# Kernel optimization log

Measured on AMD Instinct MI355X. Metric: run time of the kernel, lower is better.

The kernel has to match this reference:

```python
import jax, jax.numpy as jnp
import numpy as np

B, L = 1024, 1024
NCAT, NNUM = 20, 10
CAT_BUCKETS, SEQ_VOCAB = 100000, 50000
E, A, H, QH = 32, 128, 256, 256
TOPK = 30


def _init(key, shape, scale=0.02):
    return scale * jax.random.normal(key, shape, dtype=jnp.float32)


def setup_inputs() -> dict:
    key = jax.random.key(0)
    ks = jax.random.split(key, 24)
    z = lambda *s: jnp.zeros(s, dtype=jnp.float32)
    return {
        "cats": jax.random.randint(ks[0], (B, NCAT), 0, CAT_BUCKETS + 1),
        "nums": jax.random.normal(ks[1], (B, NNUM), dtype=jnp.float32),
        "seqs": jax.random.randint(ks[2], (B, L), 0, SEQ_VOCAB + 1),
        "tgt_ids": jax.random.randint(ks[3], (B,), 0, CAT_BUCKETS + 1),
        "cat_emb": _init(ks[4], (CAT_BUCKETS + 1, E)),
        "seq_emb": _init(ks[5], (SEQ_VOCAB + 1, E)),
        "Wnum": _init(ks[6], (NNUM, E)), "bnum": z(E),
        "Wq": _init(ks[7], (E, A)), "Wk": _init(ks[8], (E, A)), "Wv": _init(ks[9], (E, A)),
        "Wo": _init(ks[10], (A, E)), "bo": z(E),
        "Wpool": _init(ks[11], (NCAT * E, E)), "bpool": z(E),
        "Wmlp": _init(ks[12], (4 * E, H)), "bmlp": z(H),
        "q1_W1": _init(ks[13], (H, QH)), "q1_b1": z(QH),
        "q1_W2": _init(ks[14], (H, QH)), "q1_b2": z(QH),
        "q1_Wp": _init(ks[15], (QH, H)), "q1_bp": z(H),
        "q2_W1": _init(ks[16], (H, QH)), "q2_b1": z(QH),
        "q2_W2": _init(ks[17], (H, QH)), "q2_b2": z(QH),
        "q2_Wp": _init(ks[18], (QH, H)), "q2_bp": z(H),
        "Wout": _init(ks[19], (H, 1)), "bout": z(1),
    }


def _qnn(x, W1, b1, W2, b2, Wp, bp):
    # Quadratic neural block (QIN-style): Hadamard product of two linear maps,
    # projected back with a residual connection. Dropout is identity in eval.
    quad = (x @ W1 + b1) * (x @ W2 + b2)
    return x + quad @ Wp + bp


def reference(cats, nums, seqs, tgt_ids, cat_emb, seq_emb, Wnum, bnum, Wq, Wk, Wv,
              Wo, bo, Wpool, bpool, Wmlp, bmlp,
              q1_W1, q1_b1, q1_W2, q1_b2, q1_Wp, q1_bp,
              q2_W1, q2_b1, q2_W2, q2_b2, q2_Wp, q2_bp, Wout, bout):
    cat_e = cat_emb[cats]                                   # [B, NCAT, E]
    cat_pool = cat_e.reshape(cat_e.shape[0], -1) @ Wpool + bpool   # [B, E]
    num_e = nums @ Wnum + bnum                              # [B, E]
    tgt_e = cat_emb[tgt_ids]                                # [B, E] (tgt_emb shares cat_emb)
    seq_e = seq_emb[seqs]                                   # [B, L, E]

    q = tgt_e @ Wq                                          # [B, A]
    k = seq_e @ Wk                                          # [B, L, A]
    v = seq_e @ Wv                                          # [B, L, A]
    scores = jnp.einsum('ba,bla->bl', q, k) / jnp.sqrt(jnp.float32(A))

    # top-k + scatter mask + masked softmax == softmax over the top-k scores,
    # scattered implicitly via gather of the selected values.
    vals, idx = jax.lax.top_k(scores, TOPK)                 # [B, TOPK]
    w = jax.nn.softmax(vals, axis=1)                        # [B, TOPK]
    v_sel = jnp.take_along_axis(v, idx[:, :, None], axis=1)  # [B, TOPK, A]
    interest = jnp.einsum('bk,bka->ba', w, v_sel) @ Wo + bo  # [B, E]

    fused = jnp.concatenate([tgt_e, interest, cat_pool, num_e], axis=1)  # [B, 4E]
    h = jax.nn.relu(fused @ Wmlp + bmlp)                    # [B, H], dropout=eval
    h = _qnn(h, q1_W1, q1_b1, q1_W2, q1_b2, q1_Wp, q1_bp)
    h = _qnn(h, q2_W1, q2_b1, q2_W2, q2_b2, q2_Wp, q2_bp)
    return (h @ Wout + bout)[:, 0]                          # [B]
```

## Files before the change

kernel.cpp:

```cpp
#include <hip/hip_runtime.h>
#include <hip/hip_fp16.h>

#define B_ 1024
#define L_ 1024
#define NCAT_ 20
#define NNUM_ 10
#define E_ 32
#define A_ 128
#define H_ 256
#define TOPK_ 30
#define INV_SQRT_A 0.08838834764831845f

typedef _Float16 half8 __attribute__((ext_vector_type(8)));
typedef float f32x4 __attribute__((ext_vector_type(4)));

__device__ __forceinline__ unsigned sortable(float f) {
    unsigned u = __float_as_uint(f);
    return (u & 0x80000000u) ? ~u : (u | 0x80000000u);
}
__device__ __forceinline__ float unsortable(unsigned s) {
    unsigned u = (s & 0x80000000u) ? (s ^ 0x80000000u) : ~s;
    return __uint_as_float(u);
}
__device__ __forceinline__ half8 cvt_h8(const float4 u, const float4 v) {
    half8 a;
    a[0] = (_Float16)u.x; a[1] = (_Float16)u.y;
    a[2] = (_Float16)u.z; a[3] = (_Float16)u.w;
    a[4] = (_Float16)v.x; a[5] = (_Float16)v.y;
    a[6] = (_Float16)v.z; a[7] = (_Float16)v.w;
    return a;
}

#define K1_GRID 1356
__global__ __launch_bounds__(256) void fused_prep_kernel(
    const int* __restrict__ cats, const float* __restrict__ nums,
    const int* __restrict__ tgt_ids, const float* __restrict__ cat_emb,
    const float* __restrict__ Wnum, const float* __restrict__ bnum,
    const float* __restrict__ Wq, const float* __restrict__ Wk,
    const float* __restrict__ Wv, const float* __restrict__ Wo,
    const float* __restrict__ Wpool, const float* __restrict__ bpool,
    const float* __restrict__ seq_emb, const float* __restrict__ Wmlp,
    const float* __restrict__ q1W1, const float* __restrict__ q1W2,
    const float* __restrict__ q1Wp,
    const float* __restrict__ q2W1, const float* __restrict__ q2W2,
    const float* __restrict__ q2Wp,
    float* __restrict__ p_out, float* __restrict__ fused, float* __restrict__ M,
    int* __restrict__ cnt, __half2* __restrict__ seq_h2,
    __half* __restrict__ WmlpT,
    __half* __restrict__ W1T1, __half* __restrict__ W2T1, __half* __restrict__ WpT1,
    __half* __restrict__ W1T2, __half* __restrict__ W2T2, __half* __restrict__ WpT2)
{
    const int blk = blockIdx.x;
    const int t = threadIdx.x;

    if (blk < 256) {
        __shared__ float ce[4][NCAT_ * E_];
        __shared__ float tg[4][E_];
        __shared__ float nm[4][NNUM_];
        __shared__ float qs[4][A_];
        __shared__ float part[8][4][E_];
        const int r0 = blk * 4;

        for (int idx = t; idx < 640; idx += 256) {
            const int q = idx >> 3, f4 = idx & 7;
            const int row = q / 20, cat = q % 20;
            const int tok = cats[(r0 + row) * NCAT_ + cat];
            ((float4*)&ce[row][cat * 32])[f4] =
                ((const float4*)(cat_emb + (size_t)tok * 32))[f4];
        }
        if (t < 32) {
            const int row = t >> 3, f4 = t & 7;
            const int tok = tgt_ids[r0 + row];
            ((float4*)&tg[row][0])[f4] =
                ((const float4*)(cat_emb + (size_t)tok * 32))[f4];
        }
        if (t >= 64 && t < 104) {
            const int x = t - 64;
            nm[x / 10][x % 10] = nums[(r0 + x / 10) * NNUM_ + x % 10];
        }
        __syncthreads();

        {
            const int w = t >> 6, lane = t & 63;
            float q0 = 0.f, q1 = 0.f;
#pragma unroll
            for (int e = 0; e < E_; ++e) {
                float te = tg[w][e];
                q0 += te * Wq[e * A_ + lane];
                q1 += te * Wq[e * A_ + lane + 64];
            }
            qs[w][lane] = q0; qs[w][lane + 64] = q1;
        }

        {
            const int iseg = t >> 5;
            const int row = (t >> 3) & 3;
            const int c0 = (t & 7) * 4;
            float4 acc = make_float4(0.f, 0.f, 0.f, 0.f);
            const int i0 = iseg * 80;
            for (int i = i0; i < i0 + 80; ++i) {
                float4 wv = *(const float4*)(Wpool + i * 32 + c0);
                acc.x += ce[row][i] * wv.x; acc.y += ce[row][i] * wv.y;
                acc.z += ce[row][i] * wv.z; acc.w += ce[row][i] * wv.w;
            }
            *(float4*)&part[iseg][row][c0] = acc;
        }
        __syncthreads();

        if (t < 128) {
            const int row = t >> 5, c = t & 31;
            const int b = r0 + row;
            float s = bpool[c];
#pragma unroll
            for (int g = 0; g < 8; ++g) s += part[g][row][c];
            fused[b * 128 + 64 + c] = s;
            fused[b * 128 + c] = tg[row][c];

            float ne = bnum[c];
#pragma unroll
            for (int n = 0; n < NNUM_; ++n) ne += nm[row][n] * Wnum[n * 32 + c];
            fused[b * 128 + 96 + c] = ne;

            float pv = 0.f;
#pragma unroll 8
            for (int a = 0; a < A_; ++a) pv += Wk[c * A_ + a] * qs[row][a];
            p_out[b * 32 + c] = pv;
        }
        return;
    }

    if (blk < 1280) {
        int x = (blk - 256) * 256 + t;
        for (; x < 800016; x += 1024 * 256) {
            float2 v = ((const float2*)seq_emb)[x];
            seq_h2[x] = __float22half2_rn(v);
        }
        return;
    }

    if (blk < 1284) {
        if (blk == 1280 && t < 64) cnt[t] = 0;
        const int o = (blk - 1280) * 256 + t;
        const int j = o >> 5, e = o & 31;
        float sm = 0.f;
#pragma unroll 8
        for (int a = 0; a < A_; ++a) sm += Wv[j * A_ + a] * Wo[a * E_ + e];
        M[o] = sm;
        return;
    }

    {
        int c = (blk - 1284) * 256 + t;
        for (; c < 53248; c += 72 * 256) {
            const float* src; __half* dst;
            int n, k0, K;
            if (c < 4096) {
                n = c >> 4; k0 = (c & 15) << 3; K = 128;
                src = Wmlp; dst = WmlpT;
            } else {
                const int c2 = c - 4096;
                const int m = c2 >> 13, idx = c2 & 8191;
                n = idx >> 5; k0 = (idx & 31) << 3; K = 256;
                switch (m) {
                    case 0: src = q1W1; dst = W1T1; break;
                    case 1: src = q1W2; dst = W2T1; break;
                    case 2: src = q1Wp; dst = WpT1; break;
                    case 3: src = q2W1; dst = W1T2; break;
                    case 4: src = q2W2; dst = W2T2; break;
                    default: src = q2Wp; dst = WpT2; break;
                }
            }
            float v[8];
#pragma unroll
            for (int i = 0; i < 8; ++i) v[i] = src[(size_t)(k0 + i) * 256 + n];
            float4 wq;
            __half2* hp = (__half2*)&wq;
            hp[0] = __float22half2_rn(make_float2(v[0], v[1]));
            hp[1] = __float22half2_rn(make_float2(v[2], v[3]));
            hp[2] = __float22half2_rn(make_float2(v[4], v[5]));
            hp[3] = __float22half2_rn(make_float2(v[6], v[7]));
            *(float4*)(dst + (size_t)n * K + k0) = wq;
        }
    }
}

#define RM 4
#define GR 16
#define HSP 260
#define TSP 264
__global__ __launch_bounds__(512) void score_mlp_kernel(
    const int* __restrict__ seqs, const __half* __restrict__ seq_h,
    const float* __restrict__ seq_emb, const float* __restrict__ p,
    const float* __restrict__ M, const float* __restrict__ bo,
    float* __restrict__ fused, int* __restrict__ cnt,
    const __half* __restrict__ WmlpT, const float* __restrict__ bmlp,
    const __half* __restrict__ W1T1, const __half* __restrict__ W2T1,
    const __half* __restrict__ WpT1,
    const float* __restrict__ b11, const float* __restrict__ b12,
    const float* __restrict__ b1p,
    const __half* __restrict__ W1T2, const __half* __restrict__ W2T2,
    const __half* __restrict__ WpT2,
    const float* __restrict__ b21, const float* __restrict__ b22,
    const float* __restrict__ b2p,
    const float* __restrict__ Wout, const float* __restrict__ bout,
    float* __restrict__ out)
{
    const int b0 = blockIdx.x * RM;
    const int tid = threadIdx.x;

    __shared__ float sc[RM][L_];
    __shared__ float ps[RM][E_];
    __shared__ float sw[RM][32];
    __shared__ int   stok[RM][32];
    __shared__ float hs[GR][HSP];
    __shared__ __half ts_h[GR][TSP];
    __shared__ int doml;

    if (tid < RM * 32)
        ps[tid >> 5][tid & 31] = p[(b0 + (tid >> 5)) * 32 + (tid & 31)];
    __syncthreads();

    {
        const int row = tid >> 7;
        const int s = tid & 127;
        const int bb = b0 + row;
#pragma unroll
        for (int jj = 0; jj < 4; ++jj) {
            const int l1 = jj * 256 + s;
            const int l2 = l1 + 128;
            const int tok1 = seqs[bb * L_ + l1];
            const int tok2 = seqs[bb * L_ + l2];
            float4 buf[2][4];
            const float4* r1 = (const float4*)(seq_h + (size_t)tok1 * 32);
            const float4* r2 = (const float4*)(seq_h + (size_t)tok2 * 32);
#pragma unroll
            for (int i = 0; i < 4; ++i) buf[0][i] = r1[i];
#pragma unroll
            for (int i = 0; i < 4; ++i) buf[1][i] = r2[i];

            float acc0 = 0.f, acc1 = 0.f;
#pragma unroll
            for (int i = 0; i < 4; ++i) {
                const __half2* h1 = (const __half2*)&buf[0][i];
                const __half2* h2 = (const __half2*)&buf[1][i];
#pragma unroll
                for (int u = 0; u < 4; ++u) {
                    float2 f1 = __half22float2(h1[u]);
                    float2 f2 = __half22float2(h2[u]);
                    acc0 += f1.x * ps[row][i * 8 + 2 * u] + f1.y * ps[row][i * 8 + 2 * u + 1];
                    acc1 += f2.x * ps[row][i * 8 + 2 * u] + f2.y * ps[row][i * 8 + 2 * u + 1];
                }
            }
            sc[row][l1] = acc0 * INV_SQRT_A;
            sc[row][l2] = acc1 * INV_SQRT_A;
        }
    }
    __syncthreads();

    if (tid < RM * 64) {
        const int w = tid >> 6;
        const int lane = tid & 63;
        const int bb = b0 + w;

        unsigned long long key[16];
#pragma unroll
        for (int j = 0; j < 16; ++j) {
            const int l = j * 64 + lane;
            key[j] = ((unsigned long long)sortable(sc[w][l]) << 10)
                   | (unsigned)(1023 - l);
        }
#pragma unroll
        for (int a = 0; a < 15; ++a)
#pragma unroll
            for (int j = 0; j < 15 - a; ++j) {
                const bool swp = key[j] < key[j + 1];
                const unsigned long long hi = swp ? key[j + 1] : key[j];
                const unsigned long long lo = swp ? key[j] : key[j + 1];
                key[j] = hi; key[j + 1] = lo;
            }

        float myv = -1e30f; int myl = 0;
        unsigned long long front = key[0];
        for (int k = 0; k < TOPK_; ++k) {
            unsigned long long wk = front;
#pragma unroll
            for (int off = 32; off > 0; off >>= 1) {
                unsigned long long o = __shfl_xor(wk, off);
                if (o > wk) wk = o;
            }
            if (lane == k) {
                myv = unsortable((unsigned)(wk >> 10));
                myl = 1023 - (int)(wk & 1023);
            }
            if (front == wk) {
#pragma unroll
                for (int j = 0; j < 15; ++j) key[j] = key[j + 1];
                key[15] = 0ULL;
                front = key[0];
            }
        }

        float m = myv;
#pragma unroll
        for (int off = 32; off > 0; off >>= 1) m = fmaxf(m, __shfl_xor(m, off));
        float e = (lane < TOPK_) ? expf(myv - m) : 0.f;
        float s = e;
#pragma unroll
        for (int off = 32; off > 0; off >>= 1) s += __shfl_xor(s, off);
        if (lane < TOPK_) {
            sw[w][lane]   = e / s;
            stok[w][lane] = seqs[bb * L_ + myl];
        }

        if (lane < E_) {
            float acc = 0.f;
#pragma unroll
            for (int k = 0; k < TOPK_; ++k)
                acc += sw[w][k] * seq_emb[(size_t)stok[w][k] * 32 + lane];
            sc[w][lane] = acc;
        }
        if (lane < E_) {
            float acc = bo[lane];
#pragma unroll
            for (int j = 0; j < E_; ++j) acc += sc[w][j] * M[j * E_ + lane];
            fused[bb * 128 + 32 + lane] = acc;
        }
    }
    __syncthreads();

    if (tid == 0) {
        __threadfence();
        const int g = blockIdx.x >> 2;
        const int old = atomicAdd(&cnt[g], 1);
        doml = (old == 3) ? 1 : 0;
        if (old == 3) __threadfence();
    }
    __syncthreads();
    if (!doml) return;

    const int r0m = (blockIdx.x >> 2) * GR;
    const int w = tid >> 6;
    const int l = tid & 63;
    const int lr = l & 15;
    const int lk = l >> 4;
    const int n0 = w * 32;

    f32x4 hC0, hC1;
    const f32x4 zf = {0.f, 0.f, 0.f, 0.f};

    {
        half8 ax[4];
        const float* xrow = fused + (size_t)(r0m + lr) * 128 + lk * 8;
#pragma unroll
        for (int ks = 0; ks < 4; ++ks) {
            float4 u = *(const float4*)(xrow + ks * 32);
            float4 v = *(const float4*)(xrow + ks * 32 + 4);
            ax[ks] = cvt_h8(u, v);
        }
#pragma unroll
        for (int t = 0; t < 2; ++t) {
            f32x4 c = zf;
            const __half* wb = WmlpT + (size_t)(n0 + 16 * t + lr) * 128 + lk * 8;
#pragma unroll
            for (int ks = 0; ks < 4; ++ks) {
                half8 b = *(const half8*)(wb + ks * 32);
                c = __builtin_amdgcn_mfma_f32_16x16x32_f16(ax[ks], b, c, 0, 0, 0);
            }
            const int j = n0 + 16 * t + lr;
            const float bm = bmlp[j];
#pragma unroll
            for (int r = 0; r < 4; ++r) {
                float vv = fmaxf(c[r] + bm, 0.f);
                if (t == 0) hC0[r] = vv; else hC1[r] = vv;
                hs[4 * lk + r][j] = vv;
            }
        }
    }
    __syncthreads();

#pragma unroll
    for (int q = 0; q < 2; ++q) {
        const __half* W1T = q ? W1T2 : W1T1;
        const __half* W2T = q ? W2T2 : W2T1;
        const __half* WpT = q ? WpT2 : WpT1;
        const float* bb1 = q ? b21 : b11;
        const float* bb2 = q ? b22 : b12;
        const float* bbp = q ? b2p : b1p;

        half8 ah[8];
#pragma unroll
        for (int ks = 0; ks < 8; ++ks) {
            const float* hr = &hs[lr][ks * 32 + lk * 8];
            float4 u = *(const float4*)hr;
            float4 v = *(const float4*)(hr + 4);
            ah[ks] = cvt_h8(u, v);
        }
#pragma unroll
        for (int t = 0; t < 2; ++t) {
            f32x4 t1 = zf, t2 = zf;
            const __half* w1 = W1T + (size_t)(n0 + 16 * t + lr) * 256 + lk * 8;
            const __half* w2 = W2T + (size_t)(n0 + 16 * t + lr) * 256 + lk * 8;
#pragma unroll
            for (int ks = 0; ks < 8; ++ks) {
                half8 b1 = *(const half8*)(w1 + ks * 32);
                t1 = __builtin_amdgcn_mfma_f32_16x16x32_f16(ah[ks], b1, t1, 0, 0, 0);
                half8 b2 = *(const half8*)(w2 + ks * 32);
                t2 = __builtin_amdgcn_mfma_f32_16x16x32_f16(ah[ks], b2, t2, 0, 0, 0);
            }
            const int j = n0 + 16 * t + lr;
            const float v1 = bb1[j], v2 = bb2[j];
#pragma unroll
            for (int r = 0; r < 4; ++r) {
                float tv = (t1[r] + v1) * (t2[r] + v2);
                ts_h[4 * lk + r][j] = __float2half_rn(tv);
            }
        }
        __syncthreads();

        half8 pa[8];
#pragma unroll
        for (int ks = 0; ks < 8; ++ks)
            pa[ks] = *(const half8*)&ts_h[lr][ks * 32 + lk * 8];
#pragma unroll
        for (int t = 0; t < 2; ++t) {
            f32x4 c = (t == 0) ? hC0 : hC1;
            const __half* wp = WpT + (size_t)(n0 + 16 * t + lr) * 256 + lk * 8;
#pragma unroll
            for (int ks = 0; ks < 8; ++ks) {
                half8 b = *(const half8*)(wp + ks * 32);
                c = __builtin_amdgcn_mfma_f32_16x16x32_f16(pa[ks], b, c, 0, 0, 0);
            }
            const int j = n0 + 16 * t + lr;
            const float bp = bbp[j];
#pragma unroll
            for (int r = 0; r < 4; ++r) {
                float vv = c[r] + bp;
                if (t == 0) hC0[r] = vv; else hC1[r] = vv;
                hs[4 * lk + r][j] = vv;
            }
        }
        __syncthreads();
    }

    {
        const int i = tid >> 5;
        const int seg = tid & 31;
        const int cb = seg * 8;
        float psum = 0.f;
#pragma unroll
        for (int u = 0; u < 8; ++u) psum += hs[i][cb + u] * Wout[cb + u];
#pragma unroll
        for (int off = 16; off > 0; off >>= 1) psum += __shfl_xor(psum, off);
        if (seg == 0) out[r0m + i] = psum + bout[0];
    }
}

extern "C" void kernel_launch(void* const* d_in, const int* in_sizes, int n_in,
                              void* d_out, int out_size, void* d_ws, size_t ws_size,
                              hipStream_t stream) {
    const int*   cats    = (const int*)d_in[0];
    const float* nums    = (const float*)d_in[1];
    const int*   seqs    = (const int*)d_in[2];
    const int*   tgt_ids = (const int*)d_in[3];
    const float* cat_emb = (const float*)d_in[4];
    const float* seq_emb = (const float*)d_in[5];
    const float* Wnum    = (const float*)d_in[6];
    const float* bnum    = (const float*)d_in[7];
    const float* Wq      = (const float*)d_in[8];
    const float* Wk      = (const float*)d_in[9];
    const float* Wv      = (const float*)d_in[10];
    const float* Wo      = (const float*)d_in[11];
    const float* bo      = (const float*)d_in[12];
    const float* Wpool   = (const float*)d_in[13];
    const float* bpool   = (const float*)d_in[14];
    const float* Wmlp    = (const float*)d_in[15];
    const float* bmlp    = (const float*)d_in[16];
    const float* q1_W1   = (const float*)d_in[17];
    const float* q1_b1   = (const float*)d_in[18];
    const float* q1_W2   = (const float*)d_in[19];
    const float* q1_b2   = (const float*)d_in[20];
    const float* q1_Wp   = (const float*)d_in[21];
    const float* q1_bp   = (const float*)d_in[22];
    const float* q2_W1   = (const float*)d_in[23];
    const float* q2_b1   = (const float*)d_in[24];
    const float* q2_W2   = (const float*)d_in[25];
    const float* q2_b2   = (const float*)d_in[26];
    const float* q2_Wp   = (const float*)d_in[27];
    const float* q2_bp   = (const float*)d_in[28];
    const float* Wout    = (const float*)d_in[29];
    const float* bout    = (const float*)d_in[30];

    float* ws = (float*)d_ws;
    float*   p       = ws;
    float*   fused   = ws + 32768;
    float*   M       = ws + 163840;
    int*     cnt     = (int*)(ws + 164864);
    __half2* seq_h2  = (__half2*)(ws + 164928);
    __half*  WmlpT   = (__half*)(ws + 964992);
    __half*  W1T1    = (__half*)(ws + 981376);
    __half*  W2T1    = (__half*)(ws + 1014144);
    __half*  WpT1    = (__half*)(ws + 1046912);
    __half*  W1T2    = (__half*)(ws + 1079680);
    __half*  W2T2    = (__half*)(ws + 1112448);
    __half*  WpT2    = (__half*)(ws + 1145216);

    float* out = (float*)d_out;

    fused_prep_kernel<<<K1_GRID, 256, 0, stream>>>(
        cats, nums, tgt_ids, cat_emb, Wnum, bnum, Wq, Wk, Wv, Wo,
        Wpool, bpool, seq_emb, Wmlp,
        q1_W1, q1_W2, q1_Wp, q2_W1, q2_W2, q2_Wp,
        p, fused, M, cnt, seq_h2,
        WmlpT, W1T1, W2T1, WpT1, W1T2, W2T2, WpT2);

    score_mlp_kernel<<<B_ / RM, 512, 0, stream>>>(
        seqs, (const __half*)seq_h2, seq_emb, p, M, bo, fused, cnt,
        WmlpT, bmlp,
        W1T1, W2T1, WpT1, q1_b1, q1_b2, q1_bp,
        W1T2, W2T2, WpT2, q2_b1, q2_b2, q2_bp,
        Wout, bout, out);
}
```

Measured before the change: 199.3 us.

## Run MLP tail per block on its own rows instead of last-arriver grouping

Previously four score blocks combined through a global atomic counter, and only the last block to arrive ran the MFMA MLP tail on 16 rows read back from global memory. Now every block keeps its 4 fused rows in shared memory and runs the MLP tail itself, with the A-operand rows replicated (lr&3). This drops the threadfence/atomic handshake and the serialized tail, so the tail work is spread across all blocks. In exchange, each block's 16-row MFMA tiles hold only 4 distinct rows, so four times as much tile work and weight traffic is spent overall.

```diff
diff --git a/kernel.cpp b/kernel.cpp
--- a/kernel.cpp
+++ b/kernel.cpp
@@ -45,7 +45,7 @@
     const float* __restrict__ q2W1, const float* __restrict__ q2W2,
     const float* __restrict__ q2Wp,
     float* __restrict__ p_out, float* __restrict__ fused, float* __restrict__ M,
-    int* __restrict__ cnt, __half2* __restrict__ seq_h2,
+    __half2* __restrict__ seq_h2,
     __half* __restrict__ WmlpT,
     __half* __restrict__ W1T1, __half* __restrict__ W2T1, __half* __restrict__ WpT1,
     __half* __restrict__ W1T2, __half* __restrict__ W2T2, __half* __restrict__ WpT2)
@@ -139,7 +139,6 @@
     }
 
     if (blk < 1284) {
-        if (blk == 1280 && t < 64) cnt[t] = 0;
         const int o = (blk - 1280) * 256 + t;
         const int j = o >> 5, e = o & 31;
         float sm = 0.f;
@@ -188,11 +187,12 @@
 #define GR 16
 #define HSP 260
 #define TSP 264
+#define XSP 132
 __global__ __launch_bounds__(512) void score_mlp_kernel(
     const int* __restrict__ seqs, const __half* __restrict__ seq_h,
     const float* __restrict__ seq_emb, const float* __restrict__ p,
     const float* __restrict__ M, const float* __restrict__ bo,
-    float* __restrict__ fused, int* __restrict__ cnt,
+    const float* __restrict__ fused,
     const __half* __restrict__ WmlpT, const float* __restrict__ bmlp,
     const __half* __restrict__ W1T1, const __half* __restrict__ W2T1,
     const __half* __restrict__ WpT1,
@@ -212,9 +212,9 @@
     __shared__ float ps[RM][E_];
     __shared__ float sw[RM][32];
     __shared__ int   stok[RM][32];
+    __shared__ float xs[RM][XSP];
     __shared__ float hs[GR][HSP];
     __shared__ __half ts_h[GR][TSP];
-    __shared__ int doml;
 
     if (tid < RM * 32)
         ps[tid >> 5][tid & 31] = p[(b0 + (tid >> 5)) * 32 + (tid & 31)];
@@ -255,6 +255,11 @@
             sc[row][l2] = acc1 * INV_SQRT_A;
         }
     }
+    if (tid < 384) {
+        const int r = tid / 96, c0 = tid % 96;
+        const int c = (c0 < 32) ? c0 : (c0 + 32);
+        xs[r][c] = fused[(b0 + r) * 128 + c];
+    }
     __syncthreads();
 
     if (tid < RM * 64) {
@@ -323,22 +328,11 @@
             float acc = bo[lane];
 #pragma unroll
             for (int j = 0; j < E_; ++j) acc += sc[w][j] * M[j * E_ + lane];
-            fused[bb * 128 + 32 + lane] = acc;
+            xs[w][32 + lane] = acc;
         }
     }
     __syncthreads();
 
-    if (tid == 0) {
-        __threadfence();
-        const int g = blockIdx.x >> 2;
-        const int old = atomicAdd(&cnt[g], 1);
-        doml = (old == 3) ? 1 : 0;
-        if (old == 3) __threadfence();
-    }
-    __syncthreads();
-    if (!doml) return;
-
-    const int r0m = (blockIdx.x >> 2) * GR;
     const int w = tid >> 6;
     const int l = tid & 63;
     const int lr = l & 15;
@@ -350,7 +344,7 @@
 
     {
         half8 ax[4];
-        const float* xrow = fused + (size_t)(r0m + lr) * 128 + lk * 8;
+        const float* xrow = &xs[lr & 3][lk * 8];
 #pragma unroll
         for (int ks = 0; ks < 4; ++ks) {
             float4 u = *(const float4*)(xrow + ks * 32);
@@ -442,7 +436,7 @@
         __syncthreads();
     }
 
-    {
+    if (tid < 128) {
         const int i = tid >> 5;
         const int seg = tid & 31;
         const int cb = seg * 8;
@@ -451,7 +445,7 @@
         for (int u = 0; u < 8; ++u) psum += hs[i][cb + u] * Wout[cb + u];
 #pragma unroll
         for (int off = 16; off > 0; off >>= 1) psum += __shfl_xor(psum, off);
-        if (seg == 0) out[r0m + i] = psum + bout[0];
+        if (seg == 0) out[b0 + i] = psum + bout[0];
     }
 }
 
@@ -494,7 +488,6 @@
     float*   p       = ws;
     float*   fused   = ws + 32768;
     float*   M       = ws + 163840;
-    int*     cnt     = (int*)(ws + 164864);
     __half2* seq_h2  = (__half2*)(ws + 164928);
     __half*  WmlpT   = (__half*)(ws + 964992);
     __half*  W1T1    = (__half*)(ws + 981376);
@@ -510,11 +503,11 @@
         cats, nums, tgt_ids, cat_emb, Wnum, bnum, Wq, Wk, Wv, Wo,
         Wpool, bpool, seq_emb, Wmlp,
         q1_W1, q1_W2, q1_Wp, q2_W1, q2_W2, q2_Wp,
-        p, fused, M, cnt, seq_h2,
+        p, fused, M, seq_h2,
         WmlpT, W1T1, W2T1, WpT1, W1T2, W2T2, WpT2);
 
     score_mlp_kernel<<<B_ / RM, 512, 0, stream>>>(
-        seqs, (const __half*)seq_h2, seq_emb, p, M, bo, fused, cnt,
+        seqs, (const __half*)seq_h2, seq_emb, p, M, bo, fused,
         WmlpT, bmlp,
         W1T1, W2T1, WpT1, q1_b1, q1_b2, q1_bp,
         W1T2, W2T2, WpT2, q2_b1, q2_b2, q2_bp,
```

Measured after the change: 195.7 us. Within noise of the previous version (-1.8%).
